# Performance work log

Hardware: AMD Instinct MI355X
Metric: run time of the kernel (lower is better)

The kernel has to match this reference:

```python
import jax, jax.numpy as jnp
import numpy as np

N_NODES = 2_000_000
N_DAGS = 20_000
N_OBS = 1_000
DIM_EMBED = 32
NUM_NODE_FEATURES = 5
IN_DIM = NUM_NODE_FEATURES + 3 * DIM_EMBED  # 101
HIDDEN = [32, 16, 8, 1]


def _ragged_counts(rng, n_segments, total):
    # random nonnegative counts summing exactly to `total` (ragged partition)
    bounds = np.sort(rng.integers(0, total + 1, size=n_segments - 1))
    bounds = np.concatenate([[0], bounds, [total]])
    return jnp.asarray(np.diff(bounds), dtype=jnp.int64)


def setup_inputs() -> dict:
    key = jax.random.key(0)
    ks = jax.random.split(key, 16)
    rng = np.random.default_rng(0)

    inp = {
        "x": jax.random.normal(ks[0], (N_NODES, NUM_NODE_FEATURES), jnp.float32),
        "node_embeddings": jax.random.normal(ks[1], (N_NODES, DIM_EMBED), jnp.float32),
        "dag_summaries": jax.random.normal(ks[2], (N_DAGS, DIM_EMBED), jnp.float32),
        "global_summaries": jax.random.normal(ks[3], (N_OBS, DIM_EMBED), jnp.float32),
        "num_nodes_per_dag": _ragged_counts(rng, N_DAGS, N_NODES),
        "num_nodes_per_obs": _ragged_counts(rng, N_OBS, N_NODES),
        "stage_mask": jax.random.bernoulli(ks[4], 0.5, (N_NODES,)),
    }

    # MLP params: Linear(101,32) relu, Linear(32,16) relu, Linear(16,8) relu, Linear(8,1)
    dims = [IN_DIM] + HIDDEN
    for i in range(4):
        fan_in = dims[i]
        inp[f"W{i+1}"] = jax.random.normal(ks[5 + 2 * i], (dims[i], dims[i + 1]), jnp.float32) / np.sqrt(fan_in)
        inp[f"b{i+1}"] = jnp.zeros((dims[i + 1],), jnp.float32)
    return inp


def reference(x, node_embeddings, dag_summaries, global_summaries,
              num_nodes_per_dag, num_nodes_per_obs, stage_mask,
              W1, b1, W2, b2, W3, b3, W4, b4):
    n = x.shape[0]
    # ragged broadcast of per-dag / per-obs summaries to nodes
    dag_rep = jnp.repeat(dag_summaries, num_nodes_per_dag, axis=0, total_repeat_length=n)
    glob_rep = jnp.repeat(global_summaries, num_nodes_per_obs, axis=0, total_repeat_length=n)
    node_inputs = jnp.concatenate([x, node_embeddings, dag_rep, glob_rep], axis=1)  # [n, 101]

    h = jax.nn.relu(node_inputs @ W1 + b1)
    h = jax.nn.relu(h @ W2 + b2)
    h = jax.nn.relu(h @ W3 + b3)
    scores = (h @ W4 + b4)[:, 0]  # [n]

    min_real = jnp.finfo(scores.dtype).min
    return jax.nn.softmax(jnp.where(stage_mask, scores, min_real), axis=-1)
```

## Files before the change

### kernel.cpp

```cpp
#include <hip/hip_runtime.h>
#include <math.h>
#include <float.h>

#define BLK 256

__device__ __forceinline__ void scan_one(const int* __restrict__ cnt, int n,
                                         int* __restrict__ starts, int* wsum)
{
    const int t = threadIdx.x;
    const int chunk = (n + 1023) / 1024;
    const int base = t * chunk;

    int sum = 0;
    for (int k = 0; k < chunk; k++) {
        int idx = base + k;
        if (idx < n) sum += cnt[idx];
    }

    const int lane = t & 63, wid = t >> 6;
    int v = sum;
#pragma unroll
    for (int off = 1; off < 64; off <<= 1) {
        int y = __shfl_up(v, off);
        if (lane >= off) v += y;
    }
    if (lane == 63) wsum[wid] = v;
    __syncthreads();
    if (wid == 0) {
        int w = (lane < 16) ? wsum[lane] : 0;
#pragma unroll
        for (int off = 1; off < 16; off <<= 1) {
            int y = __shfl_up(w, off);
            if (lane >= off) w += y;
        }
        if (lane < 16) wsum[lane] = w;
    }
    __syncthreads();

    int thr_excl = ((wid > 0) ? wsum[wid - 1] : 0) + v - sum;
    int run = thr_excl;
    for (int k = 0; k < chunk; k++) {
        int idx = base + k;
        if (idx < n) { starts[idx] = run; run += cnt[idx]; }
    }
    if (t == 0) starts[n] = wsum[15];
    __syncthreads();
}

__global__ __launch_bounds__(1024) void scan2_kernel(
    const int* __restrict__ dag_cnt, int nd,
    const int* __restrict__ obs_cnt, int no,
    int* __restrict__ dag_starts, int* __restrict__ obs_starts)
{
    __shared__ int wsum[16];
    scan_one(dag_cnt, nd, dag_starts, wsum);
    scan_one(obs_cnt, no, obs_starts, wsum);
}

__global__ __launch_bounds__(128) void expand_ids_kernel(
    const int* __restrict__ dag_starts, int nd,
    const int* __restrict__ obs_starts, int no,
    int* __restrict__ dag_ids, int* __restrict__ obs_ids)
{
    int seg = blockIdx.x;
    if (seg < nd) {
        int s = dag_starts[seg], e = dag_starts[seg + 1];
        for (int i = s + threadIdx.x; i < e; i += 128) dag_ids[i] = seg;
    } else {
        int g = seg - nd;
        int s = obs_starts[g], e = obs_starts[g + 1];
        for (int i = s + threadIdx.x; i < e; i += 128) obs_ids[i] = g;
    }
}

__global__ __launch_bounds__(256) void seg_h1_kernel(
    const float* __restrict__ dag_sum, int nd,
    const float* __restrict__ glob_sum, int no,
    const float* __restrict__ W1, const float* __restrict__ b1,
    float* __restrict__ dag_h1, float* __restrict__ glob_h1)
{
    __shared__ float Wd[32 * 32];
    __shared__ float Wg[32 * 32];
    for (int t = threadIdx.x; t < 32 * 32; t += 256) {
        int k = t / 32, j = t % 32;
        Wd[t] = W1[(size_t)(37 + k) * 32 + j];
        Wg[t] = W1[(size_t)(69 + k) * 32 + j];
    }
    __syncthreads();

    int gid = blockIdx.x * 256 + threadIdx.x;
    int seg = gid / 32;
    int j   = gid % 32;
    if (seg >= nd + no) return;

    const float* srow;
    const float* Wl;
    float acc;
    float* outp;
    if (seg < nd) {
        srow = dag_sum + (size_t)seg * 32;
        Wl = Wd; acc = 0.f;
        outp = dag_h1 + (size_t)seg * 32 + j;
    } else {
        srow = glob_sum + (size_t)(seg - nd) * 32;
        Wl = Wg; acc = b1[j];
        outp = glob_h1 + (size_t)(seg - nd) * 32 + j;
    }
#pragma unroll
    for (int k = 0; k < 32; k++)
        acc = fmaf(srow[k], Wl[k * 32 + j], acc);
    *outp = acc;
}

__global__ __launch_bounds__(BLK) void mlp_score_kernel(
    const float* __restrict__ x, const float* __restrict__ emb,
    const float* __restrict__ dag_h1, const float* __restrict__ glob_h1,
    const int* __restrict__ dag_ids, const int* __restrict__ obs_ids,
    const int* __restrict__ mask,
    const float* __restrict__ W1, const float* __restrict__ W2,
    const float* __restrict__ b2, const float* __restrict__ W3,
    const float* __restrict__ b3, const float* __restrict__ W4,
    const float* __restrict__ b4,
    float* __restrict__ scores, float* __restrict__ blk_m,
    double* __restrict__ blk_s, int N)
{
    const int i0 = blockIdx.x * BLK + threadIdx.x;
    const bool valid = (i0 < N);
    const int i = valid ? i0 : (N - 1);

    const int d  = dag_ids[i];
    const int o  = obs_ids[i];
    const int mk = mask[i];

    const float4* dh = (const float4*)(dag_h1 + (size_t)d * 32);
    const float4* gh = (const float4*)(glob_h1 + (size_t)o * 32);
    float4 dq0 = dh[0], dq1 = dh[1], dq2 = dh[2], dq3 = dh[3],
           dq4 = dh[4], dq5 = dh[5], dq6 = dh[6], dq7 = dh[7];
    float4 gq0 = gh[0], gq1 = gh[1], gq2 = gh[2], gq3 = gh[3],
           gq4 = gh[4], gq5 = gh[5], gq6 = gh[6], gq7 = gh[7];

    const float* xr = x + (size_t)i * 5;
    float xv0 = xr[0], xv1 = xr[1], xv2 = xr[2], xv3 = xr[3], xv4 = xr[4];
    const float4* er = (const float4*)(emb + (size_t)i * 32);

    float h1[32];
#pragma unroll
    for (int c = 0; c < 4; c++) {
        h1[0  + c] = ((const float*)&dq0)[c] + ((const float*)&gq0)[c];
        h1[4  + c] = ((const float*)&dq1)[c] + ((const float*)&gq1)[c];
        h1[8  + c] = ((const float*)&dq2)[c] + ((const float*)&gq2)[c];
        h1[12 + c] = ((const float*)&dq3)[c] + ((const float*)&gq3)[c];
        h1[16 + c] = ((const float*)&dq4)[c] + ((const float*)&gq4)[c];
        h1[20 + c] = ((const float*)&dq5)[c] + ((const float*)&gq5)[c];
        h1[24 + c] = ((const float*)&dq6)[c] + ((const float*)&gq6)[c];
        h1[28 + c] = ((const float*)&dq7)[c] + ((const float*)&gq7)[c];
    }

#pragma unroll
    for (int j = 0; j < 32; j++) h1[j] = fmaf(xv0, W1[j], h1[j]);
#pragma unroll
    for (int j = 0; j < 32; j++) h1[j] = fmaf(xv1, W1[32 + j], h1[j]);
#pragma unroll
    for (int j = 0; j < 32; j++) h1[j] = fmaf(xv2, W1[64 + j], h1[j]);
#pragma unroll
    for (int j = 0; j < 32; j++) h1[j] = fmaf(xv3, W1[96 + j], h1[j]);
#pragma unroll
    for (int j = 0; j < 32; j++) h1[j] = fmaf(xv4, W1[128 + j], h1[j]);

#pragma unroll
    for (int q = 0; q < 8; q++) {
        float4 e = er[q];
#pragma unroll
        for (int kk = 0; kk < 4; kk++) {
            const int k = 5 + q * 4 + kk;
            const float v = (kk == 0) ? e.x : (kk == 1) ? e.y : (kk == 2) ? e.z : e.w;
#pragma unroll
            for (int j = 0; j < 32; j++)
                h1[j] = fmaf(v, W1[k * 32 + j], h1[j]);
        }
    }
#pragma unroll
    for (int j = 0; j < 32; j++) h1[j] = fmaxf(h1[j], 0.f);

    float h2[16];
#pragma unroll
    for (int j = 0; j < 16; j++) h2[j] = b2[j];
#pragma unroll
    for (int k = 0; k < 32; k++) {
        const float v = h1[k];
#pragma unroll
        for (int j = 0; j < 16; j++)
            h2[j] = fmaf(v, W2[k * 16 + j], h2[j]);
    }
#pragma unroll
    for (int j = 0; j < 16; j++) h2[j] = fmaxf(h2[j], 0.f);

    float h3[8];
#pragma unroll
    for (int j = 0; j < 8; j++) h3[j] = b3[j];
#pragma unroll
    for (int k = 0; k < 16; k++) {
        const float v = h2[k];
#pragma unroll
        for (int j = 0; j < 8; j++)
            h3[j] = fmaf(v, W3[k * 8 + j], h3[j]);
    }
#pragma unroll
    for (int j = 0; j < 8; j++) h3[j] = fmaxf(h3[j], 0.f);

    float s = b4[0];
#pragma unroll
    for (int k = 0; k < 8; k++) s = fmaf(h3[k], W4[k], s);

    const bool live = valid && (mk != 0);
    if (valid) scores[i0] = live ? s : -FLT_MAX;

    float  m  = live ? s : -INFINITY;
    double sd = live ? 1.0 : 0.0;
#pragma unroll
    for (int off = 32; off > 0; off >>= 1) {
        float  mo = __shfl_down(m, off);
        double so = __shfl_down(sd, off);
        float M = fmaxf(m, mo);
        double out = 0.0;
        if (m  > -INFINITY) out += sd * (double)expf(m  - M);
        if (mo > -INFINITY) out += so * (double)expf(mo - M);
        m = M; sd = out;
    }
    __shared__ float  mw[BLK / 64];
    __shared__ double sw[BLK / 64];
    const int lane = threadIdx.x & 63, wid = threadIdx.x >> 6;
    if (lane == 0) { mw[wid] = m; sw[wid] = sd; }
    __syncthreads();
    if (threadIdx.x == 0) {
        float M = mw[0]; double S = sw[0];
#pragma unroll
        for (int w = 1; w < BLK / 64; w++) {
            float mb = mw[w]; double sb = sw[w];
            float Mn = fmaxf(M, mb);
            double out = 0.0;
            if (M  > -INFINITY) out += S  * (double)expf(M  - Mn);
            if (mb > -INFINITY) out += sb * (double)expf(mb - Mn);
            M = Mn; S = out;
        }
        blk_m[blockIdx.x] = M;
        blk_s[blockIdx.x] = S;
    }
}

__global__ __launch_bounds__(1024) void merge_kernel(
    const float* __restrict__ bm, const double* __restrict__ bs, int n,
    float* __restrict__ gmax, double* __restrict__ Z)
{
    float m = -INFINITY;
    double s = 0.0;
    for (int i = threadIdx.x; i < n; i += 1024) {
        float mb = bm[i]; double sb = bs[i];
        float M = fmaxf(m, mb);
        double out = 0.0;
        if (m  > -INFINITY) out += s  * (double)expf(m  - M);
        if (mb > -INFINITY) out += sb * (double)expf(mb - M);
        m = M; s = out;
    }
    __shared__ float  mred[1024];
    __shared__ double sred[1024];
    mred[threadIdx.x] = m;
    sred[threadIdx.x] = s;
    __syncthreads();
    for (int off = 512; off > 0; off >>= 1) {
        if (threadIdx.x < off) {
            float ma = mred[threadIdx.x], mb = mred[threadIdx.x + off];
            double sa = sred[threadIdx.x], sb = sred[threadIdx.x + off];
            float M = fmaxf(ma, mb);
            double out = 0.0;
            if (ma > -INFINITY) out += sa * (double)expf(ma - M);
            if (mb > -INFINITY) out += sb * (double)expf(mb - M);
            mred[threadIdx.x] = M;
            sred[threadIdx.x] = out;
        }
        __syncthreads();
    }
    if (threadIdx.x == 0) { *gmax = mred[0]; *Z = sred[0]; }
}

__global__ __launch_bounds__(BLK) void finalize_kernel(
    const float* __restrict__ scores, int N,
    const float* __restrict__ gmaxp, const double* __restrict__ Zp,
    float* __restrict__ outp)
{
    const float gm = *gmaxp;
    const float rZ = (float)(1.0 / *Zp);
    int i = blockIdx.x * BLK + threadIdx.x;
    if (i < N) outp[i] = expf(scores[i] - gm) * rZ;
}

extern "C" void kernel_launch(void* const* d_in, const int* in_sizes, int n_in,
                              void* d_out, int out_size, void* d_ws, size_t ws_size,
                              hipStream_t stream)
{
    const float* x        = (const float*)d_in[0];
    const float* emb      = (const float*)d_in[1];
    const float* dag_sum  = (const float*)d_in[2];
    const float* glob_sum = (const float*)d_in[3];
    const int*   dag_cnt  = (const int*)d_in[4];
    const int*   obs_cnt  = (const int*)d_in[5];
    const int*   mask     = (const int*)d_in[6];
    const float* W1 = (const float*)d_in[7];
    const float* b1 = (const float*)d_in[8];
    const float* W2 = (const float*)d_in[9];
    const float* b2 = (const float*)d_in[10];
    const float* W3 = (const float*)d_in[11];
    const float* b3 = (const float*)d_in[12];
    const float* W4 = (const float*)d_in[13];
    const float* b4 = (const float*)d_in[14];
    float* outp = (float*)d_out;

    const int N  = in_sizes[0] / 5;
    const int nd = in_sizes[4];
    const int no = in_sizes[5];

    const int main_blocks = (N + BLK - 1) / BLK;

    char* ws = (char*)d_ws;
    size_t off = 0;
    auto alloc = [&](size_t bytes) {
        void* p = ws + off;
        off += (bytes + 15) & ~(size_t)15;
        return p;
    };
    int*    dag_starts = (int*)   alloc((size_t)(nd + 1) * sizeof(int));
    int*    obs_starts = (int*)   alloc((size_t)(no + 1) * sizeof(int));
    int*    dag_ids    = (int*)   alloc((size_t)N * sizeof(int));
    int*    obs_ids    = (int*)   alloc((size_t)N * sizeof(int));
    float*  dag_h1     = (float*) alloc((size_t)nd * 32 * sizeof(float));
    float*  glob_h1    = (float*) alloc((size_t)no * 32 * sizeof(float));
    float*  scores     = (float*) alloc((size_t)N * sizeof(float));
    float*  blk_m      = (float*) alloc((size_t)main_blocks * sizeof(float));
    double* blk_s      = (double*)alloc((size_t)main_blocks * sizeof(double));
    float*  gmax       = (float*) alloc(sizeof(float));
    double* Z          = (double*)alloc(sizeof(double));
    (void)ws_size;

    scan2_kernel<<<1, 1024, 0, stream>>>(dag_cnt, nd, obs_cnt, no, dag_starts, obs_starts);

    expand_ids_kernel<<<nd + no, 128, 0, stream>>>(dag_starts, nd, obs_starts, no, dag_ids, obs_ids);

    {
        int total = (nd + no) * 32;
        seg_h1_kernel<<<(total + 255) / 256, 256, 0, stream>>>(
            dag_sum, nd, glob_sum, no, W1, b1, dag_h1, glob_h1);
    }

    mlp_score_kernel<<<main_blocks, BLK, 0, stream>>>(
        x, emb, dag_h1, glob_h1, dag_ids, obs_ids, mask,
        W1, W2, b2, W3, b3, W4, b4, scores, blk_m, blk_s, N);

    merge_kernel<<<1, 1024, 0, stream>>>(blk_m, blk_s, main_blocks, gmax, Z);

    finalize_kernel<<<(N + BLK - 1) / BLK, BLK, 0, stream>>>(scores, N, gmax, Z, outp);
}
```

Measured before the change: 493.3 us.

## Make MLP score kernel persistent grid-stride with software-prefetched next-node inputs

The per-node MLP kernel now runs on a fixed grid of 1024 blocks that stride over the nodes. Each thread loads the next node's ids, mask, features and embedding while it computes the current node, and keeps a running online-softmax max and sum per thread. The reduction then merges only 1024 block partials instead of one per 256 nodes. The cost is higher register pressure from the prefetched values, which may lower occupancy. There are also fewer waves to hide latency if 1024 blocks do not fill the device.

Measured after the change: 609.8 us. 1.24x slower.

```diff
diff --git a/kernel.cpp b/kernel.cpp
--- a/kernel.cpp
+++ b/kernel.cpp
@@ -3,6 +3,7 @@
 #include <float.h>
 
 #define BLK 256
+#define K3_BLOCKS 1024
 
 __device__ __forceinline__ void scan_one(const int* __restrict__ cnt, int n,
                                          int* __restrict__ starts, int* wsum)
@@ -112,6 +113,19 @@
     *outp = acc;
 }
 
+__device__ __forceinline__ void emb4(const float4 e, const int kbase,
+                                     const float* __restrict__ W1,
+                                     float (&h1)[32])
+{
+    const float c[4] = {e.x, e.y, e.z, e.w};
+#pragma unroll
+    for (int kk = 0; kk < 4; kk++) {
+#pragma unroll
+        for (int j = 0; j < 32; j++)
+            h1[j] = fmaf(c[kk], W1[(kbase + kk) * 32 + j], h1[j]);
+    }
+}
+
 __global__ __launch_bounds__(BLK) void mlp_score_kernel(
     const float* __restrict__ x, const float* __restrict__ emb,
     const float* __restrict__ dag_h1, const float* __restrict__ glob_h1,
@@ -124,99 +138,140 @@
     float* __restrict__ scores, float* __restrict__ blk_m,
     double* __restrict__ blk_s, int N)
 {
-    const int i0 = blockIdx.x * BLK + threadIdx.x;
-    const bool valid = (i0 < N);
-    const int i = valid ? i0 : (N - 1);
-
-    const int d  = dag_ids[i];
-    const int o  = obs_ids[i];
-    const int mk = mask[i];
-
-    const float4* dh = (const float4*)(dag_h1 + (size_t)d * 32);
-    const float4* gh = (const float4*)(glob_h1 + (size_t)o * 32);
-    float4 dq0 = dh[0], dq1 = dh[1], dq2 = dh[2], dq3 = dh[3],
-           dq4 = dh[4], dq5 = dh[5], dq6 = dh[6], dq7 = dh[7];
-    float4 gq0 = gh[0], gq1 = gh[1], gq2 = gh[2], gq3 = gh[3],
-           gq4 = gh[4], gq5 = gh[5], gq6 = gh[6], gq7 = gh[7];
-
-    const float* xr = x + (size_t)i * 5;
-    float xv0 = xr[0], xv1 = xr[1], xv2 = xr[2], xv3 = xr[3], xv4 = xr[4];
-    const float4* er = (const float4*)(emb + (size_t)i * 32);
-
-    float h1[32];
-#pragma unroll
-    for (int c = 0; c < 4; c++) {
-        h1[0  + c] = ((const float*)&dq0)[c] + ((const float*)&gq0)[c];
-        h1[4  + c] = ((const float*)&dq1)[c] + ((const float*)&gq1)[c];
-        h1[8  + c] = ((const float*)&dq2)[c] + ((const float*)&gq2)[c];
-        h1[12 + c] = ((const float*)&dq3)[c] + ((const float*)&gq3)[c];
-        h1[16 + c] = ((const float*)&dq4)[c] + ((const float*)&gq4)[c];
-        h1[20 + c] = ((const float*)&dq5)[c] + ((const float*)&gq5)[c];
-        h1[24 + c] = ((const float*)&dq6)[c] + ((const float*)&gq6)[c];
-        h1[28 + c] = ((const float*)&dq7)[c] + ((const float*)&gq7)[c];
-    }
-
-#pragma unroll
-    for (int j = 0; j < 32; j++) h1[j] = fmaf(xv0, W1[j], h1[j]);
-#pragma unroll
-    for (int j = 0; j < 32; j++) h1[j] = fmaf(xv1, W1[32 + j], h1[j]);
-#pragma unroll
-    for (int j = 0; j < 32; j++) h1[j] = fmaf(xv2, W1[64 + j], h1[j]);
-#pragma unroll
-    for (int j = 0; j < 32; j++) h1[j] = fmaf(xv3, W1[96 + j], h1[j]);
-#pragma unroll
-    for (int j = 0; j < 32; j++) h1[j] = fmaf(xv4, W1[128 + j], h1[j]);
-
-#pragma unroll
-    for (int q = 0; q < 8; q++) {
-        float4 e = er[q];
-#pragma unroll
-        for (int kk = 0; kk < 4; kk++) {
-            const int k = 5 + q * 4 + kk;
-            const float v = (kk == 0) ? e.x : (kk == 1) ? e.y : (kk == 2) ? e.z : e.w;
-#pragma unroll
-            for (int j = 0; j < 32; j++)
-                h1[j] = fmaf(v, W1[k * 32 + j], h1[j]);
-        }
-    }
-#pragma unroll
-    for (int j = 0; j < 32; j++) h1[j] = fmaxf(h1[j], 0.f);
-
-    float h2[16];
-#pragma unroll
-    for (int j = 0; j < 16; j++) h2[j] = b2[j];
-#pragma unroll
-    for (int k = 0; k < 32; k++) {
-        const float v = h1[k];
-#pragma unroll
-        for (int j = 0; j < 16; j++)
-            h2[j] = fmaf(v, W2[k * 16 + j], h2[j]);
-    }
-#pragma unroll
-    for (int j = 0; j < 16; j++) h2[j] = fmaxf(h2[j], 0.f);
-
-    float h3[8];
-#pragma unroll
-    for (int j = 0; j < 8; j++) h3[j] = b3[j];
-#pragma unroll
-    for (int k = 0; k < 16; k++) {
-        const float v = h2[k];
-#pragma unroll
-        for (int j = 0; j < 8; j++)
-            h3[j] = fmaf(v, W3[k * 8 + j], h3[j]);
-    }
-#pragma unroll
-    for (int j = 0; j < 8; j++) h3[j] = fmaxf(h3[j], 0.f);
-
-    float s = b4[0];
-#pragma unroll
-    for (int k = 0; k < 8; k++) s = fmaf(h3[k], W4[k], s);
-
-    const bool live = valid && (mk != 0);
-    if (valid) scores[i0] = live ? s : -FLT_MAX;
-
-    float  m  = live ? s : -INFINITY;
-    double sd = live ? 1.0 : 0.0;
+    const int stride = gridDim.x * BLK;
+    int i = blockIdx.x * BLK + threadIdx.x;
+
+    float  m_acc = -INFINITY;
+    double s_acc = 0.0;
+
+    bool valid = (i < N);
+    const int idx0 = valid ? i : 0;
+
+    int d_  = dag_ids[idx0];
+    int o_  = obs_ids[idx0];
+    int mk_ = mask[idx0];
+    const float* xr0 = x + (size_t)idx0 * 5;
+    float x0_ = xr0[0], x1_ = xr0[1], x2_ = xr0[2], x3_ = xr0[3], x4_ = xr0[4];
+    const float4* er0 = (const float4*)(emb + (size_t)idx0 * 32);
+    float4 e0_ = er0[0], e1_ = er0[1], e2_ = er0[2], e3_ = er0[3],
+           e4_ = er0[4], e5_ = er0[5], e6_ = er0[6], e7_ = er0[7];
+
+#pragma unroll 1
+    for (; valid; ) {
+        const int  inext = i + stride;
+        const bool vnext = (inext < N);
+        const int  idxn  = vnext ? inext : i;
+
+        const float4* dh = (const float4*)(dag_h1 + (size_t)d_ * 32);
+        const float4* gh = (const float4*)(glob_h1 + (size_t)o_ * 32);
+        float4 a0 = dh[0], a1 = dh[1], a2 = dh[2], a3 = dh[3];
+        float4 p0 = gh[0], p1 = gh[1], p2 = gh[2], p3 = gh[3];
+
+        float h1[32];
+#pragma unroll
+        for (int j = 0; j < 32; j++) h1[j] = x0_ * W1[j];
+#pragma unroll
+        for (int j = 0; j < 32; j++) h1[j] = fmaf(x1_, W1[32 + j], h1[j]);
+#pragma unroll
+        for (int j = 0; j < 32; j++) h1[j] = fmaf(x2_, W1[64 + j], h1[j]);
+#pragma unroll
+        for (int j = 0; j < 32; j++) h1[j] = fmaf(x3_, W1[96 + j], h1[j]);
+#pragma unroll
+        for (int j = 0; j < 32; j++) h1[j] = fmaf(x4_, W1[128 + j], h1[j]);
+
+        emb4(e0_, 5,  W1, h1);
+        emb4(e1_, 9,  W1, h1);
+        emb4(e2_, 13, W1, h1);
+        emb4(e3_, 17, W1, h1);
+
+#pragma unroll
+        for (int c = 0; c < 4; c++) {
+            h1[0  + c] += ((const float*)&a0)[c] + ((const float*)&p0)[c];
+            h1[4  + c] += ((const float*)&a1)[c] + ((const float*)&p1)[c];
+            h1[8  + c] += ((const float*)&a2)[c] + ((const float*)&p2)[c];
+            h1[12 + c] += ((const float*)&a3)[c] + ((const float*)&p3)[c];
+        }
+
+        float4 b0v = dh[4], b1v = dh[5], b2v = dh[6], b3v = dh[7];
+        float4 q0  = gh[4], q1  = gh[5], q2  = gh[6], q3  = gh[7];
+
+        const int nd_ = dag_ids[idxn];
+        const int no_ = obs_ids[idxn];
+        const int nmk = mask[idxn];
+        const float* nxr = x + (size_t)idxn * 5;
+        const float nx0 = nxr[0], nx1 = nxr[1], nx2 = nxr[2],
+                    nx3 = nxr[3], nx4 = nxr[4];
+
+        emb4(e4_, 21, W1, h1);
+        emb4(e5_, 25, W1, h1);
+        emb4(e6_, 29, W1, h1);
+        emb4(e7_, 33, W1, h1);
+
+#pragma unroll
+        for (int c = 0; c < 4; c++) {
+            h1[16 + c] += ((const float*)&b0v)[c] + ((const float*)&q0)[c];
+            h1[20 + c] += ((const float*)&b1v)[c] + ((const float*)&q1)[c];
+            h1[24 + c] += ((const float*)&b2v)[c] + ((const float*)&q2)[c];
+            h1[28 + c] += ((const float*)&b3v)[c] + ((const float*)&q3)[c];
+        }
+
+        const float4* ner = (const float4*)(emb + (size_t)idxn * 32);
+        const float4 ne0 = ner[0], ne1 = ner[1], ne2 = ner[2], ne3 = ner[3],
+                     ne4 = ner[4], ne5 = ner[5], ne6 = ner[6], ne7 = ner[7];
+
+#pragma unroll
+        for (int j = 0; j < 32; j++) h1[j] = fmaxf(h1[j], 0.f);
+
+        float h2[16];
+#pragma unroll
+        for (int j = 0; j < 16; j++) h2[j] = b2[j];
+#pragma unroll
+        for (int k = 0; k < 32; k++) {
+            const float v = h1[k];
+#pragma unroll
+            for (int j = 0; j < 16; j++)
+                h2[j] = fmaf(v, W2[k * 16 + j], h2[j]);
+        }
+#pragma unroll
+        for (int j = 0; j < 16; j++) h2[j] = fmaxf(h2[j], 0.f);
+
+        float h3[8];
+#pragma unroll
+        for (int j = 0; j < 8; j++) h3[j] = b3[j];
+#pragma unroll
+        for (int k = 0; k < 16; k++) {
+            const float v = h2[k];
+#pragma unroll
+            for (int j = 0; j < 8; j++)
+                h3[j] = fmaf(v, W3[k * 8 + j], h3[j]);
+        }
+#pragma unroll
+        for (int j = 0; j < 8; j++) h3[j] = fmaxf(h3[j], 0.f);
+
+        float sv = b4[0];
+#pragma unroll
+        for (int k = 0; k < 8; k++) sv = fmaf(h3[k], W4[k], sv);
+
+        const bool live = (mk_ != 0);
+        scores[i] = live ? sv : -FLT_MAX;
+        if (live) {
+            if (sv <= m_acc) {
+                s_acc += (double)expf(sv - m_acc);
+            } else {
+                s_acc = s_acc * (double)expf(m_acc - sv) + 1.0;
+                m_acc = sv;
+            }
+        }
+
+        d_ = nd_; o_ = no_; mk_ = nmk;
+        x0_ = nx0; x1_ = nx1; x2_ = nx2; x3_ = nx3; x4_ = nx4;
+        e0_ = ne0; e1_ = ne1; e2_ = ne2; e3_ = ne3;
+        e4_ = ne4; e5_ = ne5; e6_ = ne6; e7_ = ne7;
+        i = inext; valid = vnext;
+    }
+
+    float  m  = m_acc;
+    double sd = s_acc;
 #pragma unroll
     for (int off = 32; off > 0; off >>= 1) {
         float  mo = __shfl_down(m, off);
@@ -319,8 +374,6 @@
     const int nd = in_sizes[4];
     const int no = in_sizes[5];
 
-    const int main_blocks = (N + BLK - 1) / BLK;
-
     char* ws = (char*)d_ws;
     size_t off = 0;
     auto alloc = [&](size_t bytes) {
@@ -335,8 +388,8 @@
     float*  dag_h1     = (float*) alloc((size_t)nd * 32 * sizeof(float));
     float*  glob_h1    = (float*) alloc((size_t)no * 32 * sizeof(float));
     float*  scores     = (float*) alloc((size_t)N * sizeof(float));
-    float*  blk_m      = (float*) alloc((size_t)main_blocks * sizeof(float));
-    double* blk_s      = (double*)alloc((size_t)main_blocks * sizeof(double));
+    float*  blk_m      = (float*) alloc((size_t)K3_BLOCKS * sizeof(float));
+    double* blk_s      = (double*)alloc((size_t)K3_BLOCKS * sizeof(double));
     float*  gmax       = (float*) alloc(sizeof(float));
     double* Z          = (double*)alloc(sizeof(double));
     (void)ws_size;
@@ -351,11 +404,11 @@
             dag_sum, nd, glob_sum, no, W1, b1, dag_h1, glob_h1);
     }
 
-    mlp_score_kernel<<<main_blocks, BLK, 0, stream>>>(
+    mlp_score_kernel<<<K3_BLOCKS, BLK, 0, stream>>>(
         x, emb, dag_h1, glob_h1, dag_ids, obs_ids, mask,
         W1, W2, b2, W3, b3, W4, b4, scores, blk_m, blk_s, N);
 
-    merge_kernel<<<1, 1024, 0, stream>>>(blk_m, blk_s, main_blocks, gmax, Z);
+    merge_kernel<<<1, 1024, 0, stream>>>(blk_m, blk_s, K3_BLOCKS, gmax, Z);
 
     finalize_kernel<<<(N + BLK - 1) / BLK, BLK, 0, stream>>>(scores, N, gmax, Z, outp);
 }
```

## Use packed fp16 dot2 instructions for per-node MLP layers

Applied to the files above, without the earlier changes.

Adds a small kernel that packs W1..W4 into fp16 pairs, and rewrites the per-node MLP to convert inputs and activations to half2 and accumulate with v_dot2 into fp32. This roughly halves the FMA instruction count and the weight loads in the compute-heavy main kernel. It adds conversion instructions and a launch, and lowers precision of inputs and weights to fp16, which can shift the softmax scores.

New measurement: 476.4 us. 1.04x faster.

```diff
diff --git a/kernel.cpp b/kernel.cpp
--- a/kernel.cpp
+++ b/kernel.cpp
@@ -3,6 +3,22 @@
 #include <float.h>
 
 #define BLK 256
+
+typedef __fp16 half2_t __attribute__((ext_vector_type(2)));
+
+static __device__ __forceinline__ half2_t pkh2(float a, float b)
+{
+    return __builtin_amdgcn_cvt_pkrtz(a, b);
+}
+
+static __device__ __forceinline__ float fdot2(half2_t a, half2_t b, float c)
+{
+#if __has_builtin(__builtin_amdgcn_fdot2)
+    return __builtin_amdgcn_fdot2(a, b, c, false);
+#else
+    return fmaf((float)a[0], (float)b[0], fmaf((float)a[1], (float)b[1], c));
+#endif
+}
 
 __device__ __forceinline__ void scan_one(const int* __restrict__ cnt, int n,
                                          int* __restrict__ starts, int* wsum)
@@ -112,14 +128,39 @@
     *outp = acc;
 }
 
+__global__ __launch_bounds__(256) void pack_weights_kernel(
+    const float* __restrict__ W1, const float* __restrict__ W2,
+    const float* __restrict__ W3, const float* __restrict__ W4,
+    half2_t* __restrict__ W1p, half2_t* __restrict__ W2p,
+    half2_t* __restrict__ W3p, half2_t* __restrict__ W4p)
+{
+    for (int t = threadIdx.x; t < 19 * 32; t += 256) {
+        int p = t / 32, j = t % 32;
+        int r0 = 2 * p, r1 = 2 * p + 1;
+        float lo = W1[(size_t)r0 * 32 + j];
+        float hi = (r1 <= 36) ? W1[(size_t)r1 * 32 + j] : 0.f;
+        W1p[t] = pkh2(lo, hi);
+    }
+    for (int t = threadIdx.x; t < 16 * 16; t += 256) {
+        int p = t / 16, j = t % 16;
+        W2p[t] = pkh2(W2[(size_t)(2 * p) * 16 + j], W2[(size_t)(2 * p + 1) * 16 + j]);
+    }
+    for (int t = threadIdx.x; t < 8 * 8; t += 256) {
+        int p = t / 8, j = t % 8;
+        W3p[t] = pkh2(W3[(size_t)(2 * p) * 8 + j], W3[(size_t)(2 * p + 1) * 8 + j]);
+    }
+    if (threadIdx.x < 4)
+        W4p[threadIdx.x] = pkh2(W4[2 * threadIdx.x], W4[2 * threadIdx.x + 1]);
+}
+
 __global__ __launch_bounds__(BLK) void mlp_score_kernel(
     const float* __restrict__ x, const float* __restrict__ emb,
     const float* __restrict__ dag_h1, const float* __restrict__ glob_h1,
     const int* __restrict__ dag_ids, const int* __restrict__ obs_ids,
     const int* __restrict__ mask,
-    const float* __restrict__ W1, const float* __restrict__ W2,
-    const float* __restrict__ b2, const float* __restrict__ W3,
-    const float* __restrict__ b3, const float* __restrict__ W4,
+    const half2_t* __restrict__ W1p, const half2_t* __restrict__ W2p,
+    const half2_t* __restrict__ W3p, const half2_t* __restrict__ W4p,
+    const float* __restrict__ b2, const float* __restrict__ b3,
     const float* __restrict__ b4,
     float* __restrict__ scores, float* __restrict__ blk_m,
     double* __restrict__ blk_s, int N)
@@ -140,77 +181,83 @@
            gq4 = gh[4], gq5 = gh[5], gq6 = gh[6], gq7 = gh[7];
 
     const float* xr = x + (size_t)i * 5;
-    float xv0 = xr[0], xv1 = xr[1], xv2 = xr[2], xv3 = xr[3], xv4 = xr[4];
+    float in_[38];
+    in_[0] = xr[0]; in_[1] = xr[1]; in_[2] = xr[2]; in_[3] = xr[3]; in_[4] = xr[4];
     const float4* er = (const float4*)(emb + (size_t)i * 32);
-
-    float h1[32];
-#pragma unroll
-    for (int c = 0; c < 4; c++) {
-        h1[0  + c] = ((const float*)&dq0)[c] + ((const float*)&gq0)[c];
-        h1[4  + c] = ((const float*)&dq1)[c] + ((const float*)&gq1)[c];
-        h1[8  + c] = ((const float*)&dq2)[c] + ((const float*)&gq2)[c];
-        h1[12 + c] = ((const float*)&dq3)[c] + ((const float*)&gq3)[c];
-        h1[16 + c] = ((const float*)&dq4)[c] + ((const float*)&gq4)[c];
-        h1[20 + c] = ((const float*)&dq5)[c] + ((const float*)&gq5)[c];
-        h1[24 + c] = ((const float*)&dq6)[c] + ((const float*)&gq6)[c];
-        h1[28 + c] = ((const float*)&dq7)[c] + ((const float*)&gq7)[c];
-    }
-
-#pragma unroll
-    for (int j = 0; j < 32; j++) h1[j] = fmaf(xv0, W1[j], h1[j]);
-#pragma unroll
-    for (int j = 0; j < 32; j++) h1[j] = fmaf(xv1, W1[32 + j], h1[j]);
-#pragma unroll
-    for (int j = 0; j < 32; j++) h1[j] = fmaf(xv2, W1[64 + j], h1[j]);
-#pragma unroll
-    for (int j = 0; j < 32; j++) h1[j] = fmaf(xv3, W1[96 + j], h1[j]);
-#pragma unroll
-    for (int j = 0; j < 32; j++) h1[j] = fmaf(xv4, W1[128 + j], h1[j]);
-
 #pragma unroll
     for (int q = 0; q < 8; q++) {
         float4 e = er[q];
-#pragma unroll
-        for (int kk = 0; kk < 4; kk++) {
-            const int k = 5 + q * 4 + kk;
-            const float v = (kk == 0) ? e.x : (kk == 1) ? e.y : (kk == 2) ? e.z : e.w;
-#pragma unroll
-            for (int j = 0; j < 32; j++)
-                h1[j] = fmaf(v, W1[k * 32 + j], h1[j]);
-        }
+        in_[5 + 4 * q + 0] = e.x;
+        in_[5 + 4 * q + 1] = e.y;
+        in_[5 + 4 * q + 2] = e.z;
+        in_[5 + 4 * q + 3] = e.w;
+    }
+    in_[37] = 0.f;
+
+    half2_t ip[19];
+#pragma unroll
+    for (int p = 0; p < 19; p++) ip[p] = pkh2(in_[2 * p], in_[2 * p + 1]);
+
+    float h1[32];
+#pragma unroll
+    for (int j = 0; j < 32; j++) h1[j] = fdot2(ip[0], W1p[j], 0.f);
+#pragma unroll
+    for (int p = 1; p < 19; p++) {
+#pragma unroll
+        for (int j = 0; j < 32; j++)
+            h1[j] = fdot2(ip[p], W1p[p * 32 + j], h1[j]);
+    }
+
+#pragma unroll
+    for (int c = 0; c < 4; c++) {
+        h1[0  + c] += ((const float*)&dq0)[c] + ((const float*)&gq0)[c];
+        h1[4  + c] += ((const float*)&dq1)[c] + ((const float*)&gq1)[c];
+        h1[8  + c] += ((const float*)&dq2)[c] + ((const float*)&gq2)[c];
+        h1[12 + c] += ((const float*)&dq3)[c] + ((const float*)&gq3)[c];
+        h1[16 + c] += ((const float*)&dq4)[c] + ((const float*)&gq4)[c];
+        h1[20 + c] += ((const float*)&dq5)[c] + ((const float*)&gq5)[c];
+        h1[24 + c] += ((const float*)&dq6)[c] + ((const float*)&gq6)[c];
+        h1[28 + c] += ((const float*)&dq7)[c] + ((const float*)&gq7)[c];
     }
 #pragma unroll
     for (int j = 0; j < 32; j++) h1[j] = fmaxf(h1[j], 0.f);
 
+    half2_t hp[16];
+#pragma unroll
+    for (int k = 0; k < 16; k++) hp[k] = pkh2(h1[2 * k], h1[2 * k + 1]);
     float h2[16];
 #pragma unroll
     for (int j = 0; j < 16; j++) h2[j] = b2[j];
 #pragma unroll
-    for (int k = 0; k < 32; k++) {
-        const float v = h1[k];
+    for (int p = 0; p < 16; p++) {
 #pragma unroll
         for (int j = 0; j < 16; j++)
-            h2[j] = fmaf(v, W2[k * 16 + j], h2[j]);
+            h2[j] = fdot2(hp[p], W2p[p * 16 + j], h2[j]);
     }
 #pragma unroll
     for (int j = 0; j < 16; j++) h2[j] = fmaxf(h2[j], 0.f);
 
+    half2_t h2p[8];
+#pragma unroll
+    for (int k = 0; k < 8; k++) h2p[k] = pkh2(h2[2 * k], h2[2 * k + 1]);
     float h3[8];
 #pragma unroll
     for (int j = 0; j < 8; j++) h3[j] = b3[j];
 #pragma unroll
-    for (int k = 0; k < 16; k++) {
-        const float v = h2[k];
+    for (int p = 0; p < 8; p++) {
 #pragma unroll
         for (int j = 0; j < 8; j++)
-            h3[j] = fmaf(v, W3[k * 8 + j], h3[j]);
+            h3[j] = fdot2(h2p[p], W3p[p * 8 + j], h3[j]);
     }
 #pragma unroll
     for (int j = 0; j < 8; j++) h3[j] = fmaxf(h3[j], 0.f);
 
+    half2_t h3p[4];
+#pragma unroll
+    for (int k = 0; k < 4; k++) h3p[k] = pkh2(h3[2 * k], h3[2 * k + 1]);
     float s = b4[0];
 #pragma unroll
-    for (int k = 0; k < 8; k++) s = fmaf(h3[k], W4[k], s);
+    for (int p = 0; p < 4; p++) s = fdot2(h3p[p], W4p[p], s);
 
     const bool live = valid && (mk != 0);
     if (valid) scores[i0] = live ? s : -FLT_MAX;
@@ -328,20 +375,26 @@
         off += (bytes + 15) & ~(size_t)15;
         return p;
     };
-    int*    dag_starts = (int*)   alloc((size_t)(nd + 1) * sizeof(int));
-    int*    obs_starts = (int*)   alloc((size_t)(no + 1) * sizeof(int));
-    int*    dag_ids    = (int*)   alloc((size_t)N * sizeof(int));
-    int*    obs_ids    = (int*)   alloc((size_t)N * sizeof(int));
-    float*  dag_h1     = (float*) alloc((size_t)nd * 32 * sizeof(float));
-    float*  glob_h1    = (float*) alloc((size_t)no * 32 * sizeof(float));
-    float*  scores     = (float*) alloc((size_t)N * sizeof(float));
-    float*  blk_m      = (float*) alloc((size_t)main_blocks * sizeof(float));
-    double* blk_s      = (double*)alloc((size_t)main_blocks * sizeof(double));
-    float*  gmax       = (float*) alloc(sizeof(float));
-    double* Z          = (double*)alloc(sizeof(double));
+    int*     dag_starts = (int*)    alloc((size_t)(nd + 1) * sizeof(int));
+    int*     obs_starts = (int*)    alloc((size_t)(no + 1) * sizeof(int));
+    int*     dag_ids    = (int*)    alloc((size_t)N * sizeof(int));
+    int*     obs_ids    = (int*)    alloc((size_t)N * sizeof(int));
+    float*   dag_h1     = (float*)  alloc((size_t)nd * 32 * sizeof(float));
+    float*   glob_h1    = (float*)  alloc((size_t)no * 32 * sizeof(float));
+    float*   scores     = (float*)  alloc((size_t)N * sizeof(float));
+    float*   blk_m      = (float*)  alloc((size_t)main_blocks * sizeof(float));
+    double*  blk_s      = (double*) alloc((size_t)main_blocks * sizeof(double));
+    float*   gmax       = (float*)  alloc(sizeof(float));
+    double*  Z          = (double*) alloc(sizeof(double));
+    half2_t* W1p        = (half2_t*)alloc((size_t)19 * 32 * sizeof(half2_t));
+    half2_t* W2p        = (half2_t*)alloc((size_t)16 * 16 * sizeof(half2_t));
+    half2_t* W3p        = (half2_t*)alloc((size_t)8 * 8 * sizeof(half2_t));
+    half2_t* W4p        = (half2_t*)alloc((size_t)4 * sizeof(half2_t));
     (void)ws_size;
 
     scan2_kernel<<<1, 1024, 0, stream>>>(dag_cnt, nd, obs_cnt, no, dag_starts, obs_starts);
+
+    pack_weights_kernel<<<1, 256, 0, stream>>>(W1, W2, W3, W4, W1p, W2p, W3p, W4p);
 
     expand_ids_kernel<<<nd + no, 128, 0, stream>>>(dag_starts, nd, obs_starts, no, dag_ids, obs_ids);
 
@@ -353,7 +406,7 @@
 
     mlp_score_kernel<<<main_blocks, BLK, 0, stream>>>(
         x, emb, dag_h1, glob_h1, dag_ids, obs_ids, mask,
-        W1, W2, b2, W3, b3, W4, b4, scores, blk_m, blk_s, N);
+        W1p, W2p, W3p, W4p, b2, b3, b4, scores, blk_m, blk_s, N);
 
     merge_kernel<<<1, 1024, 0, stream>>>(blk_m, blk_s, main_blocks, gmax, Z);
 
```
